# Kernel optimization log

Measured on AMD Instinct MI355X. Metric: run time of the kernel, lower is better.

Reference implementation:

```python
import jax, jax.numpy as jnp
import numpy as np

B, IN, OUT, COND, N, H = 512, 256, 256, 128, 8, 64
DP = max(1, int(OUT * 0.25))          # 64 periodic units (cos+sin -> 2*DP outputs)
DN = OUT - 2 * DP                     # 128 non-periodic units
TPE = IN * DP + IN * DN + DN          # params per expert
TOTAL = N * TPE


def setup_inputs() -> dict:
    key = jax.random.key(0)
    ks = jax.random.split(key, 16)
    s_in = np.sqrt(2.0 / IN).astype(np.float32)
    inp = {
        "x": jax.random.normal(ks[0], (B, IN), jnp.float32),
        "cond": jax.random.normal(ks[1], (B, COND), jnp.float32),
        # expert base weights (torch: randn * sqrt(2/in))
        "base_wp": jax.random.normal(ks[2], (N, IN, DP), jnp.float32) * s_in,
        "base_wn": jax.random.normal(ks[3], (N, IN, DN), jnp.float32) * s_in,
        "base_bn": jnp.zeros((N, DN), jnp.float32),
        # hypernet: Linear(cond,H) -> ReLU -> Linear(H, TOTAL)
        "hW1": jax.random.normal(ks[4], (COND, H), jnp.float32) / np.sqrt(COND),
        "hb1": jnp.zeros((H,), jnp.float32),
        "hW2": jax.random.normal(ks[5], (H, TOTAL), jnp.float32) / np.sqrt(H),
        "hb2": jnp.zeros((TOTAL,), jnp.float32),
        # gating: Linear(cond,3N) -> ReLU -> Linear(3N, N)
        "gW1": jax.random.normal(ks[6], (COND, 3 * N), jnp.float32) / np.sqrt(COND),
        "gb1": jnp.zeros((3 * N,), jnp.float32),
        "gW2": jax.random.normal(ks[7], (3 * N, N), jnp.float32) / np.sqrt(3 * N),
        "gb2": jnp.zeros((N,), jnp.float32),
    }
    return inp


def reference(x, cond, base_wp, base_wn, base_bn,
              hW1, hb1, hW2, hb2, gW1, gb1, gW2, gb2):
    bsz = x.shape[0]
    # hypernet -> per-sample dynamic deltas
    h = jax.nn.relu(cond @ hW1 + hb1)
    delta = (h @ hW2 + hb2).reshape(bsz, N, TPE)
    d_wp = delta[:, :, : IN * DP].reshape(bsz, N, IN, DP)
    d_wn = delta[:, :, IN * DP: IN * DP + IN * DN].reshape(bsz, N, IN, DN)
    d_bn = delta[:, :, IN * DP + IN * DN:]                  # (B, N, DN)

    # periodic branch: per-sample, per-expert mat-vec then cos/sin
    wp = base_wp[None] + d_wp                                # (B,N,IN,DP)
    per = jnp.einsum('bi,bnip->bnp', x, wp)                  # (B,N,DP)
    per_cos, per_sin = jnp.cos(per), jnp.sin(per)

    # non-periodic branch
    wn = base_wn[None] + d_wn                                # (B,N,IN,DN)
    non = jnp.einsum('bi,bnip->bnp', x, wn) + base_bn[None] + d_bn
    non = jax.nn.relu(non)                                   # (B,N,DN)

    # gating over experts
    logits = jax.nn.relu(cond @ gW1 + gb1) @ gW2 + gb2       # (B,N)
    gw = jax.nn.softmax(logits, axis=1)[:, :, None]          # (B,N,1)

    cos_c = jnp.sum(per_cos * gw, axis=1)
    sin_c = jnp.sum(per_sin * gw, axis=1)
    non_c = jnp.sum(non * gw, axis=1)
    return jnp.concatenate([cos_c, sin_c, non_c], axis=-1)   # (B, 2*DP+DN)
```

## Files before the change

kernel.cpp:

```cpp
#include <hip/hip_runtime.h>
#include <math.h>

#define BB     512
#define INF    256
#define CONDF  128
#define NEXP   8
#define HDIM   64
#define TPE    49280
#define TOTC   394240
#define NSPLIT 16
#define CW     1536
#define KB     261

#define AZ_OFF  0u
#define BTS_OFF 17104896u
#define P_OFF   18087936u
#define GW_OFF  43253760u
#define CB_OFF  43270144u

typedef __bf16          bf16x8 __attribute__((ext_vector_type(8)));
typedef unsigned short  us8    __attribute__((ext_vector_type(8)));
typedef float           f32x4  __attribute__((ext_vector_type(4)));

__device__ __forceinline__ unsigned short f2bf(float f) {
  unsigned u = __builtin_bit_cast(unsigned, f);
  u += 0x7fffu + ((u >> 16) & 1u);
  return (unsigned short)(u >> 16);
}
__device__ __forceinline__ float bf2f(unsigned short u) {
  return __builtin_bit_cast(float, ((unsigned)u) << 16);
}

__device__ __forceinline__ void gld16(const void* g, const void* l) {
  __builtin_amdgcn_global_load_lds(
      (const __attribute__((address_space(1))) unsigned int*)g,
      (__attribute__((address_space(3))) unsigned int*)l, 16, 0, 0);
}

__global__ __launch_bounds__(256, 4)
void k_prep(const float* __restrict__ hW2, unsigned short* __restrict__ Bts,
            const float* __restrict__ bwp, const float* __restrict__ bwn,
            const float* __restrict__ bbn, const float* __restrict__ hb2,
            float* __restrict__ colbias,
            const float* __restrict__ x, const float* __restrict__ cond,
            const float* __restrict__ hW1, const float* __restrict__ hb1,
            const float* __restrict__ gW1, const float* __restrict__ gb1,
            const float* __restrict__ gW2, const float* __restrict__ gb2,
            unsigned short* __restrict__ Az, float* __restrict__ gw) {
  const int bx = blockIdx.x;
  const int tid = threadIdx.x;
  __shared__ __align__(16) unsigned short Ls[64 * 256];

  if (bx < 512) {
    const int b = bx;
    float* xs  = (float*)Ls;
    float* cs  = xs + INF;
    float* hs  = cs + CONDF;
    float* g1  = hs + HDIM;
    float* lsb = g1 + 24;
    float* es  = lsb + 8;
    xs[tid] = x[b * INF + tid];
    if (tid < CONDF) cs[tid] = cond[b * CONDF + tid];
    __syncthreads();
    if (tid < HDIM) {
      float acc = hb1[tid];
      for (int q = 0; q < CONDF; ++q) acc = fmaf(cs[q], hW1[q * HDIM + tid], acc);
      hs[tid] = fmaxf(acc, 0.f);
    }
    if (tid >= 64 && tid < 88) {
      const int r = tid - 64;
      float acc = gb1[r];
      for (int q = 0; q < CONDF; ++q) acc = fmaf(cs[q], gW1[q * 24 + r], acc);
      g1[r] = fmaxf(acc, 0.f);
    }
    __syncthreads();
    if (tid < NEXP) {
      float acc = gb2[tid];
      for (int j = 0; j < 24; ++j) acc = fmaf(g1[j], gW2[j * NEXP + tid], acc);
      lsb[tid] = acc;
    }
    __syncthreads();
    if (tid < NEXP) {
      float m = lsb[0];
      for (int j = 1; j < NEXP; ++j) m = fmaxf(m, lsb[j]);
      es[tid] = expf(lsb[tid] - m);
    }
    __syncthreads();
    if (tid < NEXP) {
      float s = 0.f;
      for (int j = 0; j < NEXP; ++j) s += es[j];
      gw[b * NEXP + tid] = es[tid] / s;
    }
    const int t0 = tid >> 5, ig = tid & 31;
#pragma unroll
    for (int tt = 0; tt < 8; ++tt) {
      const int t = tt * 8 + t0;
      const float hv = hs[t];
      us8 o;
#pragma unroll
      for (int j = 0; j < 8; ++j) o[j] = f2bf(hv * xs[ig * 8 + j]);
      *(us8*)(Az + ((size_t)(t * 4 + (ig >> 3)) * BB + b) * 64 + (ig & 7) * 8) = o;
    }
    Az[((size_t)(256 + (tid >> 6)) * BB + b) * 64 + (tid & 63)] = f2bf(xs[tid]);
    if (tid < HDIM) Az[((size_t)260 * BB + b) * 64 + tid] = f2bf(hs[tid]);
    return;
  }

  if (bx >= 536) {
    const int ne = bx - 536;
    unsigned short* L2 = Ls;
#pragma unroll
    for (int it = 0; it < 8; ++it) {
      const int f = it * 256 + tid;
      const int t = f >> 5, c4 = (f & 31) * 4;
      f32x4 v = *(const f32x4*)(hW2 + (size_t)t * TOTC + (size_t)ne * TPE + 49152 + c4);
#pragma unroll
      for (int j = 0; j < 4; ++j) L2[t * 129 + c4 + j] = f2bf(v[j]);
    }
    if (tid < 192)
      colbias[ne * 192 + tid] = (tid < 64) ? 0.f
        : bbn[ne * 128 + (tid - 64)] + hb2[(size_t)ne * TPE + 49152 + (tid - 64)];
    __syncthreads();
    if (tid < 128) {
      const int c = tid;
#pragma unroll
      for (int t8 = 0; t8 < 8; ++t8) {
        us8 o;
#pragma unroll
        for (int j = 0; j < 8; ++j) o[j] = L2[(t8 * 8 + j) * 129 + c];
        *(us8*)(Bts + ((size_t)4 * CW + ne * 192 + 64 + c) * 64 + t8 * 8) = o;
      }
    } else {
      const int cz = (tid - 128) >> 1, hf = (tid - 128) & 1;
      us8 z = (us8){0, 0, 0, 0, 0, 0, 0, 0};
#pragma unroll
      for (int t8 = 0; t8 < 4; ++t8)
        *(us8*)(Bts + ((size_t)4 * CW + ne * 192 + cz) * 64 + (hf * 4 + t8) * 8) = z;
    }
    return;
  }

  const int pq = tid & 15, rg = tid >> 4, p4 = pq * 4;
  const int u = bx - 512, ne = u / 3, sec = u % 3;
  const int dst  = sec ? 128 : 64;
  const int poff = (sec == 2) ? 64 : 0;
  const int cbase = ne * 192 + sec * 64;
  const float* s1 = sec ? (bwn + (size_t)ne * INF * 128 + poff)
                        : (bwp + (size_t)ne * INF * 64);
  const float* s2 = hb2 + (size_t)ne * TPE + (sec ? 16384 : 0) + poff;
#pragma unroll
  for (int it = 0; it < 8; ++it) {
    const int i0 = rg * 2 + it * 32;
    f32x4 a1 = *(const f32x4*)(s1 + (size_t)i0 * dst + p4);
    f32x4 a2 = *(const f32x4*)(s2 + (size_t)i0 * dst + p4);
    f32x4 b1 = *(const f32x4*)(s1 + (size_t)(i0 + 1) * dst + p4);
    f32x4 b2 = *(const f32x4*)(s2 + (size_t)(i0 + 1) * dst + p4);
    const int e = i0 >> 3, q0 = i0 & 7;
#pragma unroll
    for (int j = 0; j < 4; ++j) {
      const int p = p4 + j;
      const unsigned lo = f2bf(a1[j] + a2[j]);
      const unsigned hi = f2bf(b1[j] + b2[j]);
      *(unsigned*)(&Ls[(p << 8) + (((e ^ (p >> 2)) << 3) | q0)]) = lo | (hi << 16);
    }
  }
  __syncthreads();
  us8 o[8];
#pragma unroll
  for (int it2 = 0; it2 < 8; ++it2) {
    const int of = it2 * 256 + tid;
    const int p = of >> 5, seg = of & 31;
    o[it2] = *(const us8*)(&Ls[(p << 8) + ((seg ^ (p >> 2)) << 3)]);
  }
#pragma unroll
  for (int it2 = 0; it2 < 8; ++it2) {
    const int of = it2 * 256 + tid;
    const int p = of >> 5, seg = of & 31, ib = seg >> 3, k8 = seg & 7;
    *(us8*)(Bts + ((size_t)ib * CW + cbase + p) * 64 + k8 * 8) = o[it2];
  }
}

__launch_bounds__(256, 3)
__global__ void k_gemm(const unsigned short* __restrict__ Az,
                       const float* __restrict__ hW2,
                       const unsigned short* __restrict__ Bts,
                       unsigned short* __restrict__ P) {
  const int bid = blockIdx.x;
  const int g  = (bid >> 5) * 8 + (bid & 7);
  const int mt = (bid >> 3) & 3;
  const int nt = g >> 4;
  const int s  = g & 15;
  const int m0 = mt * 128, n0 = nt * 128;
  const int kb0 = s * 16 + (s < 5 ? s : 5);
  const int kb1 = kb0 + 16 + (s < 5 ? 1 : 0);
  const int tid = threadIdx.x;
  __shared__ __align__(16) unsigned short As[128 * 64];
  __shared__ __align__(16) unsigned short Bs[128 * 64];

  f32x4 acc[4][4];
#pragma unroll
  for (int mi = 0; mi < 4; ++mi)
#pragma unroll
    for (int ni = 0; ni < 4; ++ni) acc[mi][ni] = (f32x4){0.f, 0.f, 0.f, 0.f};

  const int wv = tid >> 6, lane = tid & 63;
  const int wm = wv >> 1, wn = wv & 1;
  const int lrow = lane & 15, quad = lane >> 4;
  const int srow = tid >> 3;
  const int sg0  = tid & 7;

  const int half = tid >> 7;
  const int mq   = (tid >> 3) & 15;
  const int pi   = tid & 7;
  const int ch   = n0 + half * 64;
  const int neb  = ch / 192;
  const int r0   = ch - neb * 192;
  const int wp   = (r0 < 64);
  const int sh   = wp ? 6 : 7;
  const float* Bh = hW2 + (size_t)(neb * TPE + (wp ? r0 : 16384 + (r0 - 64)) + mq * 4);
  const int rbase = half * 64 + mq * 4;

  for (int kb = kb0; kb < kb1; ++kb) {
    const unsigned short* ab = Az + ((size_t)kb * BB + m0) * 64;
#pragma unroll
    for (int it = 0; it < 4; ++it) {
      const int r = it * 32 + srow;
      const int ga = sg0 ^ (r & 7);
      const int ldsoff = __builtin_amdgcn_readfirstlane(it * 4096 + wv * 1024);
      gld16(ab + (size_t)r * 64 + ga * 8, (const char*)As + ldsoff);
    }
    if (kb < 256) {
      const float* Br = Bh + (size_t)(kb >> 2) * TOTC;
      const int i0 = (kb & 3) * 64;
      f32x4 va[4], vb[4];
#pragma unroll
      for (int it = 0; it < 4; ++it) {
        const int ko = pi * 2 + it * 16;
        va[it] = *(const f32x4*)(Br + ((i0 + ko) << sh));
        vb[it] = *(const f32x4*)(Br + ((i0 + ko + 1) << sh));
      }
#pragma unroll
      for (int it = 0; it < 4; ++it) {
        const int gg = (pi >> 2) + it * 2;
#pragma unroll
        for (int j = 0; j < 4; ++j) {
          const int rl = rbase + j;
          const unsigned lo = f2bf(va[it][j]), hi = f2bf(vb[it][j]);
          *(unsigned*)((char*)Bs + rl * 128 + ((gg ^ (rl & 7)) << 4) + ((pi & 3) << 2))
              = lo | (hi << 16);
        }
      }
    } else {
      const unsigned short* bbp = Bts + ((size_t)(kb - 256) * CW + n0) * 64;
#pragma unroll
      for (int it = 0; it < 4; ++it) {
        const int r = it * 32 + srow;
        const int ga = sg0 ^ (r & 7);
        const int ldsoff = __builtin_amdgcn_readfirstlane(it * 4096 + wv * 1024);
        gld16(bbp + (size_t)r * 64 + ga * 8, (const char*)Bs + ldsoff);
      }
    }
    __syncthreads();
#pragma unroll
    for (int kh = 0; kh < 2; ++kh) {
      bf16x8 af[4], bfr[4];
#pragma unroll
      for (int mi = 0; mi < 4; ++mi) {
        const int r = wm * 64 + mi * 16 + lrow;
        const int ga = (kh * 4 + quad) ^ (r & 7);
        af[mi] = *(const bf16x8*)(As + r * 64 + ga * 8);
      }
#pragma unroll
      for (int ni = 0; ni < 4; ++ni) {
        const int r = wn * 64 + ni * 16 + lrow;
        const int ga = (kh * 4 + quad) ^ (r & 7);
        bfr[ni] = *(const bf16x8*)(Bs + r * 64 + ga * 8);
      }
#pragma unroll
      for (int mi = 0; mi < 4; ++mi)
#pragma unroll
        for (int ni = 0; ni < 4; ++ni)
          acc[mi][ni] = __builtin_amdgcn_mfma_f32_16x16x32_bf16(af[mi], bfr[ni], acc[mi][ni], 0, 0, 0);
    }
    __syncthreads();
  }

#pragma unroll
  for (int mi = 0; mi < 4; ++mi) {
    const int row0 = m0 + wm * 64 + mi * 16 + quad * 4;
#pragma unroll
    for (int ni = 0; ni < 4; ++ni) {
      const int col = n0 + wn * 64 + ni * 16 + lrow;
      unsigned short* pp = P + ((size_t)s * BB + row0) * CW + col;
#pragma unroll
      for (int r = 0; r < 4; ++r) pp[(size_t)r * CW] = f2bf(acc[mi][ni][r]);
    }
  }
}

__global__ void k_epi(const unsigned short* __restrict__ P, const float* __restrict__ gw,
                      const float* __restrict__ colbias, float* __restrict__ out) {
  const int b = blockIdx.x;
  const int r = threadIdx.x;
  __shared__ float gws[NEXP];
  if (r < NEXP) gws[r] = gw[b * NEXP + r];
  __syncthreads();
  float co = 0.f, si = 0.f, nc = 0.f;
  for (int n = 0; n < NEXP; ++n) {
    const int c = n * 192 + r;
    float v = colbias[c];
#pragma unroll
    for (int s2 = 0; s2 < NSPLIT; ++s2) v += bf2f(P[((size_t)s2 * BB + b) * CW + c]);
    const float g = gws[n];
    if (r < 64) { co = fmaf(g, cosf(v), co); si = fmaf(g, sinf(v), si); }
    else        { nc = fmaf(g, fmaxf(v, 0.f), nc); }
  }
  if (r < 64) { out[b * 256 + r] = co; out[b * 256 + 64 + r] = si; }
  else        { out[b * 256 + 128 + (r - 64)] = nc; }
}

extern "C" void kernel_launch(void* const* d_in, const int* in_sizes, int n_in,
                              void* d_out, int out_size, void* d_ws, size_t ws_size,
                              hipStream_t stream) {
  const float* x    = (const float*)d_in[0];
  const float* cond = (const float*)d_in[1];
  const float* bwp  = (const float*)d_in[2];
  const float* bwn  = (const float*)d_in[3];
  const float* bbn  = (const float*)d_in[4];
  const float* hW1  = (const float*)d_in[5];
  const float* hb1  = (const float*)d_in[6];
  const float* hW2  = (const float*)d_in[7];
  const float* hb2  = (const float*)d_in[8];
  const float* gW1  = (const float*)d_in[9];
  const float* gb1  = (const float*)d_in[10];
  const float* gW2  = (const float*)d_in[11];
  const float* gb2  = (const float*)d_in[12];
  float* out = (float*)d_out;
  char* ws = (char*)d_ws;

  unsigned short* Az  = (unsigned short*)(ws + AZ_OFF);
  unsigned short* Bts = (unsigned short*)(ws + BTS_OFF);
  unsigned short* Pp  = (unsigned short*)(ws + P_OFF);
  float* gw      = (float*)(ws + GW_OFF);
  float* colbias = (float*)(ws + CB_OFF);

  hipLaunchKernelGGL(k_prep, dim3(544), dim3(256), 0, stream,
                     hW2, Bts, bwp, bwn, bbn, hb2, colbias,
                     x, cond, hW1, hb1, gW1, gb1, gW2, gb2, Az, gw);
  hipLaunchKernelGGL(k_gemm, dim3(768), dim3(256), 0, stream, Az, hW2, Bts, Pp);
  hipLaunchKernelGGL(k_epi, dim3(BB), dim3(192), 0, stream, Pp, gw, colbias, out);
}
```

Before: 236.6 us.

## Double-buffer A tile and prefetch B into registers across k iterations

```diff
diff --git a/kernel.cpp b/kernel.cpp
--- a/kernel.cpp
+++ b/kernel.cpp
@@ -194,7 +194,7 @@
   const int kb0 = s * 16 + (s < 5 ? s : 5);
   const int kb1 = kb0 + 16 + (s < 5 ? 1 : 0);
   const int tid = threadIdx.x;
-  __shared__ __align__(16) unsigned short As[128 * 64];
+  __shared__ __align__(16) unsigned short As[2 * 128 * 64];
   __shared__ __align__(16) unsigned short Bs[128 * 64];
 
   f32x4 acc[4][4];
@@ -208,6 +208,7 @@
   const int lrow = lane & 15, quad = lane >> 4;
   const int srow = tid >> 3;
   const int sg0  = tid & 7;
+  const int ga_a = sg0 ^ (srow & 7);
 
   const int half = tid >> 7;
   const int mq   = (tid >> 3) & 15;
@@ -220,47 +221,75 @@
   const float* Bh = hW2 + (size_t)(neb * TPE + (wp ? r0 : 16384 + (r0 - 64)) + mq * 4);
   const int rbase = half * 64 + mq * 4;
 
-  for (int kb = kb0; kb < kb1; ++kb) {
-    const unsigned short* ab = Az + ((size_t)kb * BB + m0) * 64;
-#pragma unroll
-    for (int it = 0; it < 4; ++it) {
-      const int r = it * 32 + srow;
-      const int ga = sg0 ^ (r & 7);
-      const int ldsoff = __builtin_amdgcn_readfirstlane(it * 4096 + wv * 1024);
-      gld16(ab + (size_t)r * 64 + ga * 8, (const char*)As + ldsoff);
-    }
-    if (kb < 256) {
-      const float* Br = Bh + (size_t)(kb >> 2) * TOTC;
-      const int i0 = (kb & 3) * 64;
-      f32x4 va[4], vb[4];
-#pragma unroll
-      for (int it = 0; it < 4; ++it) {
-        const int ko = pi * 2 + it * 16;
-        va[it] = *(const f32x4*)(Br + ((i0 + ko) << sh));
-        vb[it] = *(const f32x4*)(Br + ((i0 + ko + 1) << sh));
-      }
-#pragma unroll
-      for (int it = 0; it < 4; ++it) {
-        const int gg = (pi >> 2) + it * 2;
-#pragma unroll
-        for (int j = 0; j < 4; ++j) {
-          const int rl = rbase + j;
-          const unsigned lo = f2bf(va[it][j]), hi = f2bf(vb[it][j]);
-          *(unsigned*)((char*)Bs + rl * 128 + ((gg ^ (rl & 7)) << 4) + ((pi & 3) << 2))
-              = lo | (hi << 16);
-        }
-      }
-    } else {
-      const unsigned short* bbp = Bts + ((size_t)(kb - 256) * CW + n0) * 64;
-#pragma unroll
-      for (int it = 0; it < 4; ++it) {
-        const int r = it * 32 + srow;
-        const int ga = sg0 ^ (r & 7);
-        const int ldsoff = __builtin_amdgcn_readfirstlane(it * 4096 + wv * 1024);
-        gld16(bbp + (size_t)r * 64 + ga * 8, (const char*)Bs + ldsoff);
-      }
-    }
-    __syncthreads();
+  f32x4 va[4], vb[4];
+
+#define ISSUE_A(kbn, pn)                                                      \
+  {                                                                           \
+    const unsigned short* ab = Az + ((size_t)(kbn) * BB + m0) * 64;           \
+    _Pragma("unroll")                                                         \
+    for (int it = 0; it < 4; ++it) {                                          \
+      const int r = it * 32 + srow;                                           \
+      const int ldsoff = __builtin_amdgcn_readfirstlane(                      \
+          (pn) * 16384 + it * 4096 + wv * 1024);                              \
+      gld16(ab + (size_t)r * 64 + ga_a * 8, (const char*)As + ldsoff);        \
+    }                                                                         \
+  }
+
+#define ISSUE_B(kbn)                                                          \
+  {                                                                           \
+    if ((kbn) < 256) {                                                        \
+      const float* Br = Bh + (size_t)((kbn) >> 2) * TOTC;                     \
+      const int i0 = ((kbn) & 3) * 64;                                        \
+      _Pragma("unroll")                                                       \
+      for (int it = 0; it < 4; ++it) {                                        \
+        const int ko = i0 + pi * 2 + it * 16;                                 \
+        va[it] = *(const f32x4*)(Br + ((size_t)ko << sh));                    \
+        vb[it] = *(const f32x4*)(Br + ((size_t)(ko + 1) << sh));              \
+      }                                                                       \
+    } else {                                                                  \
+      const unsigned short* bbp = Bts + ((size_t)((kbn) - 256) * CW + n0) * 64;\
+      _Pragma("unroll")                                                       \
+      for (int it = 0; it < 4; ++it)                                          \
+        va[it] = __builtin_bit_cast(                                          \
+            f32x4, *(const us8*)(bbp + (size_t)(it * 32 + srow) * 64 + ga_a * 8));\
+    }                                                                         \
+  }
+
+#define COMMIT_B(kbn)                                                         \
+  {                                                                           \
+    if ((kbn) < 256) {                                                        \
+      _Pragma("unroll")                                                       \
+      for (int it = 0; it < 4; ++it) {                                        \
+        const int gg = (pi >> 2) + it * 2;                                    \
+        _Pragma("unroll")                                                     \
+        for (int j = 0; j < 4; ++j) {                                         \
+          const int rl = rbase + j;                                           \
+          const unsigned lo = f2bf(va[it][j]), hi = f2bf(vb[it][j]);          \
+          *(unsigned*)((char*)Bs + rl * 128 + ((gg ^ (rl & 7)) << 4) +        \
+                       ((pi & 3) << 2)) = lo | (hi << 16);                    \
+        }                                                                     \
+      }                                                                       \
+    } else {                                                                  \
+      _Pragma("unroll")                                                       \
+      for (int it = 0; it < 4; ++it)                                          \
+        *(us8*)((char*)Bs + it * 4096 + tid * 16) =                           \
+            __builtin_bit_cast(us8, va[it]);                                  \
+    }                                                                         \
+  }
+
+  ISSUE_A(kb0, 0);
+  ISSUE_B(kb0);
+  COMMIT_B(kb0);
+  __syncthreads();
+
+  for (int t = kb0; t < kb1; ++t) {
+    const int p = (t - kb0) & 1;
+    const bool pf = (t + 1 < kb1);
+    if (pf) {
+      ISSUE_A(t + 1, p ^ 1);
+      ISSUE_B(t + 1);
+    }
+    const unsigned short* Asp = As + p * (128 * 64);
 #pragma unroll
     for (int kh = 0; kh < 2; ++kh) {
       bf16x8 af[4], bfr[4];
@@ -268,7 +297,7 @@
       for (int mi = 0; mi < 4; ++mi) {
         const int r = wm * 64 + mi * 16 + lrow;
         const int ga = (kh * 4 + quad) ^ (r & 7);
-        af[mi] = *(const bf16x8*)(As + r * 64 + ga * 8);
+        af[mi] = *(const bf16x8*)(Asp + r * 64 + ga * 8);
       }
 #pragma unroll
       for (int ni = 0; ni < 4; ++ni) {
@@ -283,7 +312,14 @@
           acc[mi][ni] = __builtin_amdgcn_mfma_f32_16x16x32_bf16(af[mi], bfr[ni], acc[mi][ni], 0, 0, 0);
     }
     __syncthreads();
-  }
+    if (pf) {
+      COMMIT_B(t + 1);
+      __syncthreads();
+    }
+  }
+#undef ISSUE_A
+#undef ISSUE_B
+#undef COMMIT_B
 
 #pragma unroll
   for (int mi = 0; mi < 4; ++mi) {
```

Result: faster. 230.0 us (-2.8%).
